# Performance work log

Hardware: AMD Instinct MI355X
Metric: run time of the kernel (lower is better)

## Reference

```python
import jax, jax.numpy as jnp
import numpy as np

N = 16384      # nodes
E = 524288     # edges (avg degree 32)
D = 128        # node_dim
H = 256        # hidden_dim
C = 10         # num_classes
G = 64         # graphs in batch


def setup_inputs() -> dict:
    key = jax.random.key(0)
    ks = jax.random.split(key, 8)
    x = jax.random.normal(ks[0], (N, D), dtype=jnp.float32)
    edge_index = jax.random.randint(ks[1], (2, E), 0, N)
    batch = jnp.sort(jax.random.randint(ks[2], (N,), 0, G))
    s = 0.05
    W1 = jax.random.normal(ks[3], (D, H), dtype=jnp.float32) * s
    b1 = jnp.zeros((H,), dtype=jnp.float32)
    W2 = jax.random.normal(ks[4], (H, H), dtype=jnp.float32) * s
    b2 = jnp.zeros((H,), dtype=jnp.float32)
    Wc = jax.random.normal(ks[5], (H, C), dtype=jnp.float32) * s
    bc = jnp.zeros((C,), dtype=jnp.float32)
    return {"x": x, "edge_index": edge_index, "batch": batch,
            "W1": W1, "b1": b1, "W2": W2, "b2": b2, "Wc": Wc, "bc": bc}


def _adj_norm(edge_index, n, dtype):
    # dense adjacency with self-loops (duplicates collapse to 1 via .set),
    # symmetric degree normalization D^{-1/2} A D^{-1/2}
    adj = jnp.zeros((n, n), dtype=dtype)
    adj = adj.at[edge_index[0], edge_index[1]].set(1.0)
    diag = jnp.arange(n)
    adj = adj.at[diag, diag].set(1.0)
    deg = jnp.clip(adj.sum(axis=1), 1.0, None)
    dis = deg ** -0.5
    return dis[:, None] * adj * dis[None, :]


def reference(x, edge_index, batch, W1, b1, W2, b2, Wc, bc):
    n = x.shape[0]
    A = _adj_norm(edge_index, n, x.dtype)   # [n, n], same for both layers
    h = jax.nn.relu((A @ x) @ W1 + b1)      # GCN layer 1 + relu
    h = jax.nn.relu((A @ h) @ W2 + b2)      # GCN layer 2 + relu
    pooled = jax.ops.segment_sum(h, batch, num_segments=G)            # [G, H]
    counts = jax.ops.segment_sum(jnp.ones((n,), h.dtype), batch, num_segments=G)
    pooled = pooled / jnp.clip(counts, 1.0, None)[:, None]
    # dropout is identity in eval mode
    return pooled @ Wc + bc                  # [G, C]
```

## Files before the change

kernel.cpp:

```cpp
#include <hip/hip_runtime.h>
#include <hip/hip_fp16.h>

#define NN 16384
#define EE 524288
#define DDIM 128
#define HDIM 256
#define CDIM 10
#define GG 64
#define MAXD 128

typedef _Float16 h8 __attribute__((ext_vector_type(8)));
typedef float f4 __attribute__((ext_vector_type(4)));
typedef unsigned short su8 __attribute__((ext_vector_type(8)));

#define OFF_XH   0ull
#define OFF_ELL  4194304ull
#define OFF_ELLP 8388608ull
#define OFF_Y1H  16777216ull
#define OFF_H1   20971520ull
#define OFF_Y2H  29360128ull
#define OFF_DEG  37748736ull
#define OFF_DIS  37814272ull
#define OFF_POOL 37879808ull
#define OFF_CNT  37945344ull
#define OFF_WT1  37949440ull
#define OFF_WT2  38014976ull

__global__ void init_all(const float* __restrict__ x, _Float16* __restrict__ xh,
                         const float* __restrict__ W1, _Float16* __restrict__ wt1,
                         const float* __restrict__ W2, _Float16* __restrict__ wt2,
                         unsigned short* __restrict__ ell, int* __restrict__ deg,
                         float* __restrict__ pooled, float* __restrict__ cnt,
                         const int* __restrict__ batch) {
    int b = blockIdx.x, t = threadIdx.x;
    if (b < 2048) {
        int i = (b * 256 + t) * 4;
        float4 v = *(const float4*)(x + i);
        _Float16 o[4] = {(_Float16)v.x, (_Float16)v.y, (_Float16)v.z, (_Float16)v.w};
        *(ushort4*)(xh + i) = *(ushort4*)o;
    } else if (b < 2176) {
        int i = (b - 2048) * 256 + t;
        int n = i / DDIM, k = i - n * DDIM;
        wt1[i] = (_Float16)W1[k * 256 + n];
    } else if (b < 2432) {
        int i = (b - 2176) * 256 + t;
        int n = i / HDIM, k = i - n * HDIM;
        wt2[i] = (_Float16)W2[k * 256 + n];
    } else {
        int r = (b - 2432) * 256 + t;
        deg[r] = 1;
        ell[r * MAXD] = (unsigned short)r;
        pooled[r] = 0.0f;
        if (r < GG) {
            int lo = 0, hi = NN;
            while (lo < hi) { int m = (lo + hi) >> 1; if (batch[m] < r) lo = m + 1; else hi = m; }
            int a = lo;
            lo = 0; hi = NN;
            while (lo < hi) { int m = (lo + hi) >> 1; if (batch[m] < r + 1) lo = m + 1; else hi = m; }
            cnt[r] = (float)(lo - a);
        }
    }
}

__global__ void edge_append(const int* __restrict__ ei, unsigned short* __restrict__ ell,
                            int* __restrict__ deg) {
    int e = (blockIdx.x * 256 + threadIdx.x) * 2;
    int2 s2 = *(const int2*)(ei + e);
    int2 d2 = *(const int2*)(ei + EE + e);
    int pos = atomicAdd(&deg[s2.x], 1);
    if (pos < MAXD) ell[s2.x * MAXD + pos] = (unsigned short)d2.x;
    pos = atomicAdd(&deg[s2.y], 1);
    if (pos < MAXD) ell[s2.y * MAXD + pos] = (unsigned short)d2.y;
}

__global__ __launch_bounds__(256) void dedup_kernel(unsigned short* __restrict__ ell,
                                                    int* __restrict__ deg,
                                                    float* __restrict__ dis) {
    int row  = blockIdx.x * 4 + (threadIdx.x >> 6);
    int lane = threadIdx.x & 63;
    int d = deg[row];
    if (d > MAXD) d = MAXD;
    int c0 = ell[row * MAXD + lane];
    int c1 = ell[row * MAXD + 64 + lane];
    bool k0 = lane < d;
    bool k1 = (64 + lane) < d;
    for (int j = 0; j < d - 1; j++) {
        int cj0 = __shfl(c0, j & 63, 64);
        int cj1 = __shfl(c1, j & 63, 64);
        int cj = (j < 64) ? cj0 : cj1;
        if (k0 && lane > j && c0 == cj) k0 = false;
        if (k1 && (64 + lane) > j && c1 == cj) k1 = false;
    }
    unsigned long long m0 = __ballot(k0);
    unsigned long long m1 = __ballot(k1);
    int nd = __popcll(m0) + __popcll(m1);
    unsigned long long below = (lane == 0) ? 0ull : ((~0ull) >> (64 - lane));
    int p0 = __popcll(m0 & below);
    int p1 = __popcll(m0) + __popcll(m1 & below);
    if (k0) ell[row * MAXD + p0] = (unsigned short)c0;
    if (k1) ell[row * MAXD + p1] = (unsigned short)c1;
    if (lane == 0) {
        deg[row] = nd;
        dis[row] = 1.0f / sqrtf((float)nd);
    }
}

__global__ void pack_kernel(const unsigned short* __restrict__ ell,
                            const int* __restrict__ deg, const float* __restrict__ dis,
                            unsigned* __restrict__ ellp) {
    int i = blockIdx.x * 256 + threadIdx.x;
    int row = i >> 7;
    int slot = i & 127;
    int c = ell[i] & (NN - 1);
    float w = (slot < deg[row]) ? dis[c] : 0.0f;
    _Float16 wh = (_Float16)w;
    ellp[i] = (unsigned)c | ((unsigned)(*(unsigned short*)&wh) << 16);
}

template <int COLS>
__global__ __launch_bounds__(256) void spmm_f16(const _Float16* __restrict__ src,
                                                const unsigned* __restrict__ ellp,
                                                const int* __restrict__ deg,
                                                const float* __restrict__ dis,
                                                _Float16* __restrict__ y) {
    constexpr int SEG = COLS / 8;
    constexpr int NS  = 64 / SEG;
    constexpr int ST  = 2 * NS;
    __shared__ unsigned scw[2][MAXD];
    __shared__ float red[2][ST][COLS];
    const int row0 = blockIdx.x * 2;
    const int t    = threadIdx.x;
    const int wv   = t >> 6;
    const int ri   = wv >> 1;
    const int wp   = wv & 1;
    const int lane = t & 63;
    const int sid  = lane / SEG;
    const int l    = lane % SEG;
    const int row  = row0 + ri;
    if (t < 2 * MAXD) scw[t >> 7][t & 127] = ellp[(size_t)(row0 + (t >> 7)) * MAXD + (t & 127)];
    __syncthreads();
    const int d = deg[row];

    float acc[8];
#pragma unroll
    for (int j = 0; j < 8; j++) acc[j] = 0.0f;

    const int stream = wp * NS + sid;
#pragma unroll 4
    for (int k = stream; k < d; k += ST) {
        unsigned u = scw[ri][k];
        int col = u & 0xFFFF;
        unsigned short wb = (unsigned short)(u >> 16);
        float wgt = (float)(*(_Float16*)&wb);
        su8 hv = *(const su8*)(src + (size_t)col * COLS + l * 8);
#pragma unroll
        for (int j = 0; j < 8; j++) {
            unsigned short hb = hv[j];
            acc[j] = fmaf(wgt, (float)(*(_Float16*)&hb), acc[j]);
        }
    }
    *(f4*)&red[ri][stream][l * 8]     = (f4){acc[0], acc[1], acc[2], acc[3]};
    *(f4*)&red[ri][stream][l * 8 + 4] = (f4){acc[4], acc[5], acc[6], acc[7]};
    __syncthreads();
    if (COLS == 256) {
        float s0 = 0.0f, s1 = 0.0f;
#pragma unroll
        for (int q = 0; q < ST; q++) { s0 += red[0][q][t & (COLS - 1)]; s1 += red[1][q][t & (COLS - 1)]; }
        y[(size_t)row0 * COLS + (t & (COLS - 1))]       = (_Float16)(dis[row0] * s0);
        y[(size_t)(row0 + 1) * COLS + (t & (COLS - 1))] = (_Float16)(dis[row0 + 1] * s1);
    } else {
        int rr = t >> 7, c = t & 127;
        float s = 0.0f;
#pragma unroll
        for (int q = 0; q < ST; q++) s += red[rr][q][c];
        y[(size_t)(row0 + rr) * COLS + c] = (_Float16)(dis[row0 + rr] * s);
    }
}

#define ASTR 40
#define BSTR 40

#define MFMA_PROLOG                                                            \
    const int r0 = blockIdx.x * 128;                                           \
    const int c0 = blockIdx.y * 64;                                            \
    const int t = threadIdx.x;                                                 \
    const int lane = t & 63, wv = t >> 6;                                      \
    const int wm = wv >> 1, wn = wv & 1;                                       \
    const int qm = lane & 15, qk = lane >> 4;                                  \
    f4 acc[4][2];                                                              \
    _Pragma("unroll") for (int i = 0; i < 4; i++)                              \
        _Pragma("unroll") for (int j = 0; j < 2; j++)                          \
            acc[i][j] = (f4){0.f, 0.f, 0.f, 0.f};

#define MFMA_KLOOP(Aptr, Wtptr, K)                                             \
    for (int k0 = 0; k0 < K; k0 += 32) {                                       \
        __syncthreads();                                                       \
        {                                                                      \
            int r = t >> 1, ko = (t & 1) * 16;                                 \
            const su8* srcA = (const su8*)(Aptr + (size_t)(r0 + r) * K + k0 + ko); \
            su8 a0 = srcA[0], a1 = srcA[1];                                    \
            *(su8*)&As[r * ASTR + ko]     = a0;                                \
            *(su8*)&As[r * ASTR + ko + 8] = a1;                                \
            int n = t >> 2, ko2 = (t & 3) * 8;                                 \
            *(su8*)&Bs[n * BSTR + ko2] =                                       \
                *(const su8*)(Wtptr + (size_t)(c0 + n) * K + k0 + ko2);        \
        }                                                                      \
        __syncthreads();                                                       \
        h8 bfr[2];                                                             \
        _Pragma("unroll") for (int j = 0; j < 2; j++)                          \
            bfr[j] = *(const h8*)&Bs[(wn * 32 + j * 16 + qm) * BSTR + qk * 8]; \
        _Pragma("unroll") for (int i = 0; i < 4; i++) {                        \
            h8 afr = *(const h8*)&As[(wm * 64 + i * 16 + qm) * ASTR + qk * 8]; \
            _Pragma("unroll") for (int j = 0; j < 2; j++)                      \
                acc[i][j] = __builtin_amdgcn_mfma_f32_16x16x32_f16(            \
                    afr, bfr[j], acc[i][j], 0, 0, 0);                          \
        }                                                                      \
    }

template <int K>
__global__ __launch_bounds__(256) void gemm_mfma_f16(
        const _Float16* __restrict__ A, const _Float16* __restrict__ Wt,
        const float* __restrict__ bias, _Float16* __restrict__ H) {
    __shared__ __align__(16) _Float16 As[128 * ASTR];
    __shared__ __align__(16) _Float16 Bs[64 * BSTR];
    __shared__ __align__(16) _Float16 Cs[128 * 72];
    MFMA_PROLOG
    MFMA_KLOOP(A, Wt, K)

    float bv[2];
#pragma unroll
    for (int j = 0; j < 2; j++) bv[j] = bias[c0 + wn * 32 + j * 16 + qm];
#pragma unroll
    for (int i = 0; i < 4; i++)
#pragma unroll
        for (int j = 0; j < 2; j++) {
            int lc = wn * 32 + j * 16 + qm;
#pragma unroll
            for (int rr = 0; rr < 4; rr++) {
                int lr = wm * 64 + i * 16 + qk * 4 + rr;
                Cs[lr * 72 + lc] = (_Float16)fmaxf(acc[i][j][rr] + bv[j], 0.0f);
            }
        }
    __syncthreads();
    {
        int r = t >> 1, half_ = t & 1;
        _Float16* dst = H + (size_t)(r0 + r) * 256 + c0 + half_ * 32;
        const _Float16* srcc = &Cs[r * 72 + half_ * 32];
#pragma unroll
        for (int q = 0; q < 4; q++)
            *(su8*)(dst + q * 8) = *(const su8*)(srcc + q * 8);
    }
}

#define NG 8
template <int K>
__global__ __launch_bounds__(256) void gemm_mfma_pool(
        const _Float16* __restrict__ A, const _Float16* __restrict__ Wt,
        const float* __restrict__ bias, const int* __restrict__ batch,
        float* __restrict__ pooled) {
    __shared__ __align__(16) _Float16 As[128 * ASTR];
    __shared__ __align__(16) _Float16 Bs[64 * BSTR];
    __shared__ float pools[NG][68];
    __shared__ int sb[128];
    MFMA_PROLOG
    if (t < 128) sb[t] = batch[r0 + t];
    for (int i = t; i < NG * 68; i += 256) ((float*)pools)[i] = 0.0f;
    MFMA_KLOOP(A, Wt, K)

    float bv[2];
#pragma unroll
    for (int j = 0; j < 2; j++) bv[j] = bias[c0 + wn * 32 + j * 16 + qm];
    __syncthreads();
    const int g0 = sb[0];
#pragma unroll
    for (int i = 0; i < 4; i++)
#pragma unroll
        for (int j = 0; j < 2; j++) {
            int lc = wn * 32 + j * 16 + qm;
#pragma unroll
            for (int rr = 0; rr < 4; rr++) {
                int lr = wm * 64 + i * 16 + qk * 4 + rr;
                int gi = min(sb[lr] - g0, NG - 1);
                float v = fmaxf(acc[i][j][rr] + bv[j], 0.0f);
                atomicAdd(&pools[gi][lc], v);
            }
        }
    __syncthreads();
    const int ng = min(sb[127] - g0 + 1, NG);
    for (int i2 = t; i2 < ng * 64; i2 += 256) {
        int gi = i2 >> 6, c = i2 & 63;
        float v = pools[gi][c];
        if (v != 0.0f) atomicAdd(&pooled[(g0 + gi) * 256 + c0 + c], v);
    }
}

__global__ void head_kernel(const float* __restrict__ pooled,
                            const float* __restrict__ cnt,
                            const float* __restrict__ Wc,
                            const float* __restrict__ bc,
                            float* __restrict__ out) {
    int g = blockIdx.x;
    int l = threadIdx.x;
    float inv = 1.0f / fmaxf(cnt[g], 1.0f);
    float acc[CDIM];
#pragma unroll
    for (int c = 0; c < CDIM; c++) acc[c] = 0.0f;
    for (int t = l; t < 256; t += 64) {
        float pv = pooled[g * 256 + t] * inv;
#pragma unroll
        for (int c = 0; c < CDIM; c++) acc[c] = fmaf(pv, Wc[t * CDIM + c], acc[c]);
    }
#pragma unroll
    for (int c = 0; c < CDIM; c++) {
        float v = acc[c];
        for (int off = 32; off > 0; off >>= 1) v += __shfl_down(v, off, 64);
        if (l == 0) out[g * CDIM + c] = v + bc[c];
    }
}

extern "C" void kernel_launch(void* const* d_in, const int* in_sizes, int n_in,
                              void* d_out, int out_size, void* d_ws, size_t ws_size,
                              hipStream_t stream) {
    const float* x  = (const float*)d_in[0];
    const int*   ei = (const int*)d_in[1];
    const int*   batch = (const int*)d_in[2];
    const float* W1 = (const float*)d_in[3];
    const float* b1 = (const float*)d_in[4];
    const float* W2 = (const float*)d_in[5];
    const float* b2 = (const float*)d_in[6];
    const float* Wc = (const float*)d_in[7];
    const float* bc = (const float*)d_in[8];
    float* out = (float*)d_out;

    char* ws = (char*)d_ws;
    _Float16* xh   = (_Float16*)(ws + OFF_XH);
    unsigned short* ell = (unsigned short*)(ws + OFF_ELL);
    unsigned* ellp = (unsigned*)(ws + OFF_ELLP);
    _Float16* y1h  = (_Float16*)(ws + OFF_Y1H);
    _Float16* h1   = (_Float16*)(ws + OFF_H1);
    _Float16* y2h  = (_Float16*)(ws + OFF_Y2H);
    int*   deg     = (int*)(ws + OFF_DEG);
    float* dis     = (float*)(ws + OFF_DIS);
    float* pooled  = (float*)(ws + OFF_POOL);
    float* cnt     = (float*)(ws + OFF_CNT);
    _Float16* wt1  = (_Float16*)(ws + OFF_WT1);
    _Float16* wt2  = (_Float16*)(ws + OFF_WT2);

    init_all<<<2496, 256, 0, stream>>>(x, xh, W1, wt1, W2, wt2, ell, deg,
                                       pooled, cnt, batch);
    edge_append<<<EE / 512, 256, 0, stream>>>(ei, ell, deg);
    dedup_kernel<<<NN / 4, 256, 0, stream>>>(ell, deg, dis);
    pack_kernel<<<(NN * MAXD) / 256, 256, 0, stream>>>(ell, deg, dis, ellp);
    spmm_f16<DDIM><<<NN / 2, 256, 0, stream>>>(xh, ellp, deg, dis, y1h);
    {
        dim3 grid(NN / 128, 256 / 64);
        gemm_mfma_f16<DDIM><<<grid, 256, 0, stream>>>(y1h, wt1, b1, h1);
    }
    spmm_f16<HDIM><<<NN / 2, 256, 0, stream>>>(h1, ellp, deg, dis, y2h);
    {
        dim3 grid(NN / 128, 256 / 64);
        gemm_mfma_pool<HDIM><<<grid, 256, 0, stream>>>(y2h, wt2, b2, batch, pooled);
    }
    head_kernel<<<GG, 64, 0, stream>>>(pooled, cnt, Wc, bc, out);
}
```

Measured before the change: 213.8 us.

## Fuse edge append into init kernel and prefetch next gather row in SpMM

Folds the edge-append scatter into the init kernel: deg is zeroed by a memset, the self-loop is implied in slot 0 and injected during dedup. The SpMM inner loop is restructured to software-prefetch the next neighbor row while accumulating the current one, with the trip count padded to the stream count. Padding relies on the packed ELL entries beyond the degree being zero-weighted, and it adds extra gathers for low-degree rows.

```diff
diff --git a/kernel.cpp b/kernel.cpp
--- a/kernel.cpp
+++ b/kernel.cpp
@@ -29,7 +29,8 @@
 __global__ void init_all(const float* __restrict__ x, _Float16* __restrict__ xh,
                          const float* __restrict__ W1, _Float16* __restrict__ wt1,
                          const float* __restrict__ W2, _Float16* __restrict__ wt2,
-                         unsigned short* __restrict__ ell, int* __restrict__ deg,
+                         const int* __restrict__ ei, unsigned short* __restrict__ ell,
+                         int* __restrict__ deg,
                          float* __restrict__ pooled, float* __restrict__ cnt,
                          const int* __restrict__ batch) {
     int b = blockIdx.x, t = threadIdx.x;
@@ -46,10 +47,8 @@
         int i = (b - 2176) * 256 + t;
         int n = i / HDIM, k = i - n * HDIM;
         wt2[i] = (_Float16)W2[k * 256 + n];
-    } else {
+    } else if (b < 2496) {
         int r = (b - 2432) * 256 + t;
-        deg[r] = 1;
-        ell[r * MAXD] = (unsigned short)r;
         pooled[r] = 0.0f;
         if (r < GG) {
             int lo = 0, hi = NN;
@@ -59,18 +58,15 @@
             while (lo < hi) { int m = (lo + hi) >> 1; if (batch[m] < r + 1) lo = m + 1; else hi = m; }
             cnt[r] = (float)(lo - a);
         }
-    }
-}
-
-__global__ void edge_append(const int* __restrict__ ei, unsigned short* __restrict__ ell,
-                            int* __restrict__ deg) {
-    int e = (blockIdx.x * 256 + threadIdx.x) * 2;
-    int2 s2 = *(const int2*)(ei + e);
-    int2 d2 = *(const int2*)(ei + EE + e);
-    int pos = atomicAdd(&deg[s2.x], 1);
-    if (pos < MAXD) ell[s2.x * MAXD + pos] = (unsigned short)d2.x;
-    pos = atomicAdd(&deg[s2.y], 1);
-    if (pos < MAXD) ell[s2.y * MAXD + pos] = (unsigned short)d2.y;
+    } else {
+        int e = ((b - 2496) * 256 + t) * 2;
+        int2 s2 = *(const int2*)(ei + e);
+        int2 d2 = *(const int2*)(ei + EE + e);
+        int pos = atomicAdd(&deg[s2.x], 1) + 1;
+        if (pos < MAXD) ell[s2.x * MAXD + pos] = (unsigned short)d2.x;
+        pos = atomicAdd(&deg[s2.y], 1) + 1;
+        if (pos < MAXD) ell[s2.y * MAXD + pos] = (unsigned short)d2.y;
+    }
 }
 
 __global__ __launch_bounds__(256) void dedup_kernel(unsigned short* __restrict__ ell,
@@ -78,9 +74,9 @@
                                                     float* __restrict__ dis) {
     int row  = blockIdx.x * 4 + (threadIdx.x >> 6);
     int lane = threadIdx.x & 63;
-    int d = deg[row];
+    int d = deg[row] + 1;
     if (d > MAXD) d = MAXD;
-    int c0 = ell[row * MAXD + lane];
+    int c0 = (lane == 0) ? row : ell[row * MAXD + lane];
     int c1 = ell[row * MAXD + 64 + lane];
     bool k0 = lane < d;
     bool k1 = (64 + lane) < d;
@@ -139,25 +135,33 @@
     const int row  = row0 + ri;
     if (t < 2 * MAXD) scw[t >> 7][t & 127] = ellp[(size_t)(row0 + (t >> 7)) * MAXD + (t & 127)];
     __syncthreads();
-    const int d = deg[row];
+    const int d    = deg[row];
+    const int dpad = (d + ST - 1) & ~(ST - 1);
 
     float acc[8];
 #pragma unroll
     for (int j = 0; j < 8; j++) acc[j] = 0.0f;
 
     const int stream = wp * NS + sid;
-#pragma unroll 4
-    for (int k = stream; k < d; k += ST) {
-        unsigned u = scw[ri][k];
-        int col = u & 0xFFFF;
-        unsigned short wb = (unsigned short)(u >> 16);
+    unsigned ucur = scw[ri][stream];
+    su8 hcur = *(const su8*)(src + (size_t)(ucur & 0xFFFF) * COLS + l * 8);
+    for (int k = stream; k < dpad; k += ST) {
+        const int kn = k + ST;
+        unsigned unext = 0;
+        su8 hnext;
+        if (kn < dpad) {
+            unext = scw[ri][kn];
+            hnext = *(const su8*)(src + (size_t)(unext & 0xFFFF) * COLS + l * 8);
+        }
+        unsigned short wb = (unsigned short)(ucur >> 16);
         float wgt = (float)(*(_Float16*)&wb);
-        su8 hv = *(const su8*)(src + (size_t)col * COLS + l * 8);
 #pragma unroll
         for (int j = 0; j < 8; j++) {
-            unsigned short hb = hv[j];
+            unsigned short hb = hcur[j];
             acc[j] = fmaf(wgt, (float)(*(_Float16*)&hb), acc[j]);
         }
+        ucur = unext;
+        hcur = hnext;
     }
     *(f4*)&red[ri][stream][l * 8]     = (f4){acc[0], acc[1], acc[2], acc[3]};
     *(f4*)&red[ri][stream][l * 8 + 4] = (f4){acc[4], acc[5], acc[6], acc[7]};
@@ -165,9 +169,9 @@
     if (COLS == 256) {
         float s0 = 0.0f, s1 = 0.0f;
 #pragma unroll
-        for (int q = 0; q < ST; q++) { s0 += red[0][q][t & (COLS - 1)]; s1 += red[1][q][t & (COLS - 1)]; }
-        y[(size_t)row0 * COLS + (t & (COLS - 1))]       = (_Float16)(dis[row0] * s0);
-        y[(size_t)(row0 + 1) * COLS + (t & (COLS - 1))] = (_Float16)(dis[row0 + 1] * s1);
+        for (int q = 0; q < ST; q++) { s0 += red[0][q][t]; s1 += red[1][q][t]; }
+        y[(size_t)row0 * COLS + t]       = (_Float16)(dis[row0] * s0);
+        y[(size_t)(row0 + 1) * COLS + t] = (_Float16)(dis[row0 + 1] * s1);
     } else {
         int rr = t >> 7, c = t & 127;
         float s = 0.0f;
@@ -346,9 +350,9 @@
     _Float16* wt1  = (_Float16*)(ws + OFF_WT1);
     _Float16* wt2  = (_Float16*)(ws + OFF_WT2);
 
-    init_all<<<2496, 256, 0, stream>>>(x, xh, W1, wt1, W2, wt2, ell, deg,
+    hipMemsetAsync(deg, 0, NN * sizeof(int), stream);
+    init_all<<<3520, 256, 0, stream>>>(x, xh, W1, wt1, W2, wt2, ei, ell, deg,
                                        pooled, cnt, batch);
-    edge_append<<<EE / 512, 256, 0, stream>>>(ei, ell, deg);
     dedup_kernel<<<NN / 4, 256, 0, stream>>>(ell, deg, dis);
     pack_kernel<<<(NN * MAXD) / 256, 256, 0, stream>>>(ell, deg, dis, ellp);
     spmm_f16<DDIM><<<NN / 2, 256, 0, stream>>>(xh, ellp, deg, dis, y1h);
```

After: 217.0 us. Within noise of the previous version (+1.5%).

## Fuse edge append into init kernel and process four rows per SpMM block

Applied to the files above, without the earlier changes.

The edge-append pass now runs as extra blocks inside init_all. Degree is zeroed by a memset, and the self-loop is injected in dedup as slot 0, with edges written at atomic position +1. The SpMM kernels now use 512-thread blocks that each handle four rows instead of two, which halves the block count and gives a generic reduction loop. This removes one kernel launch and its serialization, at the cost of an added memset and larger shared memory per block.

```diff
diff --git a/kernel.cpp b/kernel.cpp
--- a/kernel.cpp
+++ b/kernel.cpp
@@ -29,7 +29,8 @@
 __global__ void init_all(const float* __restrict__ x, _Float16* __restrict__ xh,
                          const float* __restrict__ W1, _Float16* __restrict__ wt1,
                          const float* __restrict__ W2, _Float16* __restrict__ wt2,
-                         unsigned short* __restrict__ ell, int* __restrict__ deg,
+                         const int* __restrict__ ei, unsigned short* __restrict__ ell,
+                         int* __restrict__ deg,
                          float* __restrict__ pooled, float* __restrict__ cnt,
                          const int* __restrict__ batch) {
     int b = blockIdx.x, t = threadIdx.x;
@@ -46,10 +47,8 @@
         int i = (b - 2176) * 256 + t;
         int n = i / HDIM, k = i - n * HDIM;
         wt2[i] = (_Float16)W2[k * 256 + n];
-    } else {
+    } else if (b < 2496) {
         int r = (b - 2432) * 256 + t;
-        deg[r] = 1;
-        ell[r * MAXD] = (unsigned short)r;
         pooled[r] = 0.0f;
         if (r < GG) {
             int lo = 0, hi = NN;
@@ -59,18 +58,15 @@
             while (lo < hi) { int m = (lo + hi) >> 1; if (batch[m] < r + 1) lo = m + 1; else hi = m; }
             cnt[r] = (float)(lo - a);
         }
-    }
-}
-
-__global__ void edge_append(const int* __restrict__ ei, unsigned short* __restrict__ ell,
-                            int* __restrict__ deg) {
-    int e = (blockIdx.x * 256 + threadIdx.x) * 2;
-    int2 s2 = *(const int2*)(ei + e);
-    int2 d2 = *(const int2*)(ei + EE + e);
-    int pos = atomicAdd(&deg[s2.x], 1);
-    if (pos < MAXD) ell[s2.x * MAXD + pos] = (unsigned short)d2.x;
-    pos = atomicAdd(&deg[s2.y], 1);
-    if (pos < MAXD) ell[s2.y * MAXD + pos] = (unsigned short)d2.y;
+    } else {
+        int e = ((b - 2496) * 256 + t) * 2;
+        int2 s2 = *(const int2*)(ei + e);
+        int2 d2 = *(const int2*)(ei + EE + e);
+        int pos = atomicAdd(&deg[s2.x], 1) + 1;
+        if (pos < MAXD) ell[s2.x * MAXD + pos] = (unsigned short)d2.x;
+        pos = atomicAdd(&deg[s2.y], 1) + 1;
+        if (pos < MAXD) ell[s2.y * MAXD + pos] = (unsigned short)d2.y;
+    }
 }
 
 __global__ __launch_bounds__(256) void dedup_kernel(unsigned short* __restrict__ ell,
@@ -78,9 +74,9 @@
                                                     float* __restrict__ dis) {
     int row  = blockIdx.x * 4 + (threadIdx.x >> 6);
     int lane = threadIdx.x & 63;
-    int d = deg[row];
+    int d = deg[row] + 1;
     if (d > MAXD) d = MAXD;
-    int c0 = ell[row * MAXD + lane];
+    int c0 = (lane == 0) ? row : ell[row * MAXD + lane];
     int c1 = ell[row * MAXD + 64 + lane];
     bool k0 = lane < d;
     bool k1 = (64 + lane) < d;
@@ -118,7 +114,7 @@
 }
 
 template <int COLS>
-__global__ __launch_bounds__(256) void spmm_f16(const _Float16* __restrict__ src,
+__global__ __launch_bounds__(512) void spmm_f16(const _Float16* __restrict__ src,
                                                 const unsigned* __restrict__ ellp,
                                                 const int* __restrict__ deg,
                                                 const float* __restrict__ dis,
@@ -126,9 +122,9 @@
     constexpr int SEG = COLS / 8;
     constexpr int NS  = 64 / SEG;
     constexpr int ST  = 2 * NS;
-    __shared__ unsigned scw[2][MAXD];
-    __shared__ float red[2][ST][COLS];
-    const int row0 = blockIdx.x * 2;
+    __shared__ unsigned scw[4][MAXD];
+    __shared__ float red[4][ST][COLS];
+    const int row0 = blockIdx.x * 4;
     const int t    = threadIdx.x;
     const int wv   = t >> 6;
     const int ri   = wv >> 1;
@@ -137,7 +133,7 @@
     const int sid  = lane / SEG;
     const int l    = lane % SEG;
     const int row  = row0 + ri;
-    if (t < 2 * MAXD) scw[t >> 7][t & 127] = ellp[(size_t)(row0 + (t >> 7)) * MAXD + (t & 127)];
+    scw[t >> 7][t & 127] = ellp[(size_t)(row0 + (t >> 7)) * MAXD + (t & 127)];
     __syncthreads();
     const int d = deg[row];
 
@@ -162,14 +158,8 @@
     *(f4*)&red[ri][stream][l * 8]     = (f4){acc[0], acc[1], acc[2], acc[3]};
     *(f4*)&red[ri][stream][l * 8 + 4] = (f4){acc[4], acc[5], acc[6], acc[7]};
     __syncthreads();
-    if (COLS == 256) {
-        float s0 = 0.0f, s1 = 0.0f;
-#pragma unroll
-        for (int q = 0; q < ST; q++) { s0 += red[0][q][t & (COLS - 1)]; s1 += red[1][q][t & (COLS - 1)]; }
-        y[(size_t)row0 * COLS + (t & (COLS - 1))]       = (_Float16)(dis[row0] * s0);
-        y[(size_t)(row0 + 1) * COLS + (t & (COLS - 1))] = (_Float16)(dis[row0 + 1] * s1);
-    } else {
-        int rr = t >> 7, c = t & 127;
+    for (int o = t; o < 4 * COLS; o += 512) {
+        int rr = o / COLS, c = o % COLS;
         float s = 0.0f;
 #pragma unroll
         for (int q = 0; q < ST; q++) s += red[rr][q][c];
@@ -346,17 +336,17 @@
     _Float16* wt1  = (_Float16*)(ws + OFF_WT1);
     _Float16* wt2  = (_Float16*)(ws + OFF_WT2);
 
-    init_all<<<2496, 256, 0, stream>>>(x, xh, W1, wt1, W2, wt2, ell, deg,
+    hipMemsetAsync(deg, 0, NN * sizeof(int), stream);
+    init_all<<<3520, 256, 0, stream>>>(x, xh, W1, wt1, W2, wt2, ei, ell, deg,
                                        pooled, cnt, batch);
-    edge_append<<<EE / 512, 256, 0, stream>>>(ei, ell, deg);
     dedup_kernel<<<NN / 4, 256, 0, stream>>>(ell, deg, dis);
     pack_kernel<<<(NN * MAXD) / 256, 256, 0, stream>>>(ell, deg, dis, ellp);
-    spmm_f16<DDIM><<<NN / 2, 256, 0, stream>>>(xh, ellp, deg, dis, y1h);
+    spmm_f16<DDIM><<<NN / 4, 512, 0, stream>>>(xh, ellp, deg, dis, y1h);
     {
         dim3 grid(NN / 128, 256 / 64);
         gemm_mfma_f16<DDIM><<<grid, 256, 0, stream>>>(y1h, wt1, b1, h1);
     }
-    spmm_f16<HDIM><<<NN / 2, 256, 0, stream>>>(h1, ellp, deg, dis, y2h);
+    spmm_f16<HDIM><<<NN / 4, 512, 0, stream>>>(h1, ellp, deg, dis, y2h);
     {
         dim3 grid(NN / 128, 256 / 64);
         gemm_mfma_pool<HDIM><<<grid, 256, 0, stream>>>(y2h, wt2, b2, batch, pooled);
```

After: 213.0 us. Within noise of the previous version (-0.4%).
